# Kernel optimization log

Hardware: AMD Instinct MI355X
Metric: run time of the kernel (lower is better)

The kernel has to match this reference:

```python
import jax, jax.numpy as jnp
import numpy as np

B, S, H = 2, 2048, 1024
NH, HD = 16, 64  # num heads, head dim
EPS = 1e-12


def setup_inputs() -> dict:
    key = jax.random.key(0)
    ks = jax.random.split(key, 10)
    sc = 1.0 / np.sqrt(H)
    return {
        "hidden_states": jax.random.normal(ks[0], (B, S, H), jnp.float32),
        "Wq": jax.random.normal(ks[1], (H, H), jnp.float32) * sc,
        "bq": jnp.zeros((H,), jnp.float32),
        "Wk": jax.random.normal(ks[2], (H, H), jnp.float32) * sc,
        "bk": jnp.zeros((H,), jnp.float32),
        "Wv": jax.random.normal(ks[3], (H, H), jnp.float32) * sc,
        "bv": jnp.zeros((H,), jnp.float32),
        "Wo": jax.random.normal(ks[4], (H, H), jnp.float32) * sc,
        "bo": jnp.zeros((H,), jnp.float32),
        "ln_g": jnp.ones((H,), jnp.float32),
        "ln_b": jnp.zeros((H,), jnp.float32),
    }


def reference(hidden_states, Wq, bq, Wk, bk, Wv, bv, Wo, bo, ln_g, ln_b):
    x = hidden_states  # [B,S,H]
    def split_heads(t):
        return t.reshape(B, S, NH, HD).transpose(0, 2, 1, 3)  # [B,NH,S,HD]
    q = split_heads(x @ Wq.T + bq)
    k = split_heads(x @ Wk.T + bk)
    v = split_heads(x @ Wv.T + bv)
    scores = jnp.einsum("bhqd,bhkd->bhqk", q, k) / np.sqrt(HD)
    causal = jnp.tril(jnp.ones((S, S), bool))  # [S,S]
    scores = jnp.where(causal[None, None], scores, -jnp.inf)
    probs = jax.nn.softmax(scores, axis=-1)
    ctx = jnp.einsum("bhqk,bhkd->bhqd", probs, v)
    ctx = ctx.transpose(0, 2, 1, 3).reshape(B, S, H)
    attn_out = ctx @ Wo.T + bo
    y = attn_out + x
    mu = jnp.mean(y, axis=-1, keepdims=True)
    var = jnp.mean((y - mu) ** 2, axis=-1, keepdims=True)
    return (y - mu) / jnp.sqrt(var + EPS) * ln_g + ln_b
```

## Files before the change

kernel.cpp:

```cpp
#include <hip/hip_runtime.h>

#define B_  2
#define S_  2048
#define H_  1024
#define NH_ 16
#define HD_ 64
#define M_  (B_*S_)

typedef __attribute__((ext_vector_type(8))) __bf16 bf16x8;
typedef __attribute__((ext_vector_type(4))) float  f32x4;
typedef __attribute__((ext_vector_type(8))) unsigned short us8;
typedef __attribute__((ext_vector_type(4))) float  fl4;

__device__ __forceinline__ unsigned short f2bf(float f) {
    unsigned int u = __float_as_uint(f);
    u += 0x7fffu + ((u >> 16) & 1u);
    return (unsigned short)(u >> 16);
}

__global__ __launch_bounds__(256) void cast_kernel(
    const float* __restrict__ x,
    const float* __restrict__ wq, const float* __restrict__ wk,
    const float* __restrict__ wv, const float* __restrict__ wo,
    unsigned short* __restrict__ xb, unsigned short* __restrict__ wb) {
    size_t t  = (size_t)blockIdx.x * 256 + threadIdx.x;
    size_t e0 = t * 4;
    const size_t XN = (size_t)M_ * H_;
    const float* src;
    unsigned short* dst;
    if (e0 < XN) { src = x + e0; dst = xb + e0; }
    else {
        size_t j = e0 - XN;
        int w = (int)(j >> 20);
        size_t off = j & ((1u << 20) - 1);
        const float* wp = (w == 0) ? wq : (w == 1) ? wk : (w == 2) ? wv : wo;
        src = wp + off; dst = wb + j;
    }
    fl4 v = *(const fl4*)src;
    ushort4 o;
    o.x = f2bf(v.x); o.y = f2bf(v.y); o.z = f2bf(v.z); o.w = f2bf(v.w);
    *(ushort4*)dst = o;
}

__global__ __launch_bounds__(512) void gemm_qkv(
    const unsigned short* __restrict__ xb, const unsigned short* __restrict__ wb,
    const float* __restrict__ bq, const float* __restrict__ bk,
    const float* __restrict__ bv,
    unsigned short* __restrict__ qb, unsigned short* __restrict__ kbuf,
    unsigned short* __restrict__ vT) {
    __shared__ __align__(16) unsigned short As[128 * 72];
    __shared__ __align__(16) unsigned short Bs[128 * 72];
    const int z = blockIdx.z;
    const unsigned short* W = wb + ((size_t)z << 20);
    const int m0 = blockIdx.x * 128, n0 = blockIdx.y * 128;
    const int t = threadIdx.x, lane = t & 63, w = t >> 6;
    const int wm = w >> 2, wn = w & 3;
    const int quad = lane >> 4, l16 = lane & 15;
    const int sr = t >> 2, sc = (t & 3) * 16;
    const unsigned short* ga = xb + (size_t)(m0 + sr) * H_ + sc;
    const unsigned short* gb = W  + (size_t)(n0 + sr) * H_ + sc;

    us8 a0 = *(const us8*)(ga),     a1 = *(const us8*)(ga + 8);
    us8 b0 = *(const us8*)(gb),     b1 = *(const us8*)(gb + 8);

    f32x4 acc[4][2] = {};
    for (int k0 = 0; k0 < H_; k0 += 64) {
        if (k0) __syncthreads();
        *(us8*)&As[sr * 72 + sc]     = a0;  *(us8*)&As[sr * 72 + sc + 8] = a1;
        *(us8*)&Bs[sr * 72 + sc]     = b0;  *(us8*)&Bs[sr * 72 + sc + 8] = b1;
        __syncthreads();
        if (k0 + 64 < H_) {
            ga += 64; gb += 64;
            a0 = *(const us8*)(ga);  a1 = *(const us8*)(ga + 8);
            b0 = *(const us8*)(gb);  b1 = *(const us8*)(gb + 8);
        }
#pragma unroll
        for (int kk = 0; kk < 64; kk += 32) {
            bf16x8 af[4], bfr[2];
#pragma unroll
            for (int i = 0; i < 4; i++)
                af[i]  = *(const bf16x8*)&As[(wm * 64 + i * 16 + l16) * 72 + kk + quad * 8];
#pragma unroll
            for (int jn = 0; jn < 2; jn++)
                bfr[jn] = *(const bf16x8*)&Bs[(wn * 32 + jn * 16 + l16) * 72 + kk + quad * 8];
#pragma unroll
            for (int mi = 0; mi < 4; mi++)
#pragma unroll
                for (int ni = 0; ni < 2; ni++)
                    acc[mi][ni] = __builtin_amdgcn_mfma_f32_16x16x32_bf16(
                        af[mi], bfr[ni], acc[mi][ni], 0, 0, 0);
        }
    }
    const float* bias = (z == 0) ? bq : (z == 1) ? bk : bv;
    if (z == 2) {
#pragma unroll
        for (int mi = 0; mi < 4; mi++) {
#pragma unroll
            for (int ni = 0; ni < 2; ni++) {
                int col  = n0 + wn * 32 + ni * 16 + l16;
                float bval = bias[col];
                int row0 = m0 + wm * 64 + mi * 16 + quad * 4;
                int bb = row0 >> 11, s0 = row0 & 2047;
                ushort4 pk;
                pk.x = f2bf(acc[mi][ni][0] + bval);
                pk.y = f2bf(acc[mi][ni][1] + bval);
                pk.z = f2bf(acc[mi][ni][2] + bval);
                pk.w = f2bf(acc[mi][ni][3] + bval);
                *(ushort4*)&vT[((size_t)bb * NH_ * HD_ + col) * S_ + s0] = pk;
            }
        }
    } else {
        unsigned short* out = (z == 0) ? qb : kbuf;
        const float qs = (z == 0) ? 0.18033688f : 1.0f;
#pragma unroll
        for (int mi = 0; mi < 4; mi++) {
#pragma unroll
            for (int ni = 0; ni < 2; ni++) {
                int col = n0 + wn * 32 + ni * 16 + l16;
                float bval = bias[col];
#pragma unroll
                for (int r = 0; r < 4; r++) {
                    int row = m0 + wm * 64 + mi * 16 + quad * 4 + r;
                    out[(size_t)row * H_ + col] = f2bf((acc[mi][ni][r] + bval) * qs);
                }
            }
        }
    }
}

__global__ __launch_bounds__(512) void gemm_out(
    const unsigned short* __restrict__ ctxb, const unsigned short* __restrict__ wob,
    const float* __restrict__ bo, const float* __restrict__ x,
    float* __restrict__ y) {
    __shared__ __align__(16) unsigned short As[128 * 72];
    __shared__ __align__(16) unsigned short Bs[128 * 72];
    const int m0 = blockIdx.x * 128, n0 = blockIdx.y * 128;
    const int t = threadIdx.x, lane = t & 63, w = t >> 6;
    const int wm = w >> 2, wn = w & 3;
    const int quad = lane >> 4, l16 = lane & 15;
    const int sr = t >> 2, sc = (t & 3) * 16;
    const unsigned short* ga = ctxb + (size_t)(m0 + sr) * H_ + sc;
    const unsigned short* gb = wob  + (size_t)(n0 + sr) * H_ + sc;

    us8 a0 = *(const us8*)(ga),     a1 = *(const us8*)(ga + 8);
    us8 b0 = *(const us8*)(gb),     b1 = *(const us8*)(gb + 8);

    f32x4 acc[4][2] = {};
    for (int k0 = 0; k0 < H_; k0 += 64) {
        if (k0) __syncthreads();
        *(us8*)&As[sr * 72 + sc]     = a0;  *(us8*)&As[sr * 72 + sc + 8] = a1;
        *(us8*)&Bs[sr * 72 + sc]     = b0;  *(us8*)&Bs[sr * 72 + sc + 8] = b1;
        __syncthreads();
        if (k0 + 64 < H_) {
            ga += 64; gb += 64;
            a0 = *(const us8*)(ga);  a1 = *(const us8*)(ga + 8);
            b0 = *(const us8*)(gb);  b1 = *(const us8*)(gb + 8);
        }
#pragma unroll
        for (int kk = 0; kk < 64; kk += 32) {
            bf16x8 af[4], bfr[2];
#pragma unroll
            for (int i = 0; i < 4; i++)
                af[i]  = *(const bf16x8*)&As[(wm * 64 + i * 16 + l16) * 72 + kk + quad * 8];
#pragma unroll
            for (int jn = 0; jn < 2; jn++)
                bfr[jn] = *(const bf16x8*)&Bs[(wn * 32 + jn * 16 + l16) * 72 + kk + quad * 8];
#pragma unroll
            for (int mi = 0; mi < 4; mi++)
#pragma unroll
                for (int ni = 0; ni < 2; ni++)
                    acc[mi][ni] = __builtin_amdgcn_mfma_f32_16x16x32_bf16(
                        af[mi], bfr[ni], acc[mi][ni], 0, 0, 0);
        }
    }
#pragma unroll
    for (int mi = 0; mi < 4; mi++) {
#pragma unroll
        for (int ni = 0; ni < 2; ni++) {
            int col = n0 + wn * 32 + ni * 16 + l16;
            float bval = bo[col];
#pragma unroll
            for (int r = 0; r < 4; r++) {
                size_t idx = (size_t)(m0 + wm * 64 + mi * 16 + quad * 4 + r) * H_ + col;
                y[idx] = acc[mi][ni][r] + bval + x[idx];
            }
        }
    }
}

__global__ __launch_bounds__(512, 4) void attn_kernel(
    const unsigned short* __restrict__ qb, const unsigned short* __restrict__ kb,
    const unsigned short* __restrict__ vT, unsigned short* __restrict__ ctxb) {
    __shared__ __align__(16) unsigned short Ks[2][64 * 72];
    __shared__ __align__(16) unsigned short Vt[2][64 * 72];
    __shared__ __align__(16) unsigned short Ps[128 * 76];
    const int flat = blockIdx.x;
    const int xcd = flat & 7, slot = flat >> 3;
    const int bh  = xcd * 4 + (slot >> 4);
    const int p   = slot & 15;
    const int b = bh >> 4, h = bh & 15;
    const int t = threadIdx.x, lane = t & 63, wid = t >> 6;
    const int grp = wid >> 2, wid4 = wid & 3;
    const int quad = lane >> 4, l16 = lane & 15;
    const int sr8 = t >> 3, sc8 = (t & 7) * 8;
    const size_t headoff = (size_t)h * HD_;
    const unsigned short* vtb = vT + ((size_t)(b * NH_ + h) * HD_) * S_;

    const int qt = grp ? (31 - p) : p;
    const int q0 = qt * 64;
    const int nsteps = 32 - p;

    const size_t qr = (size_t)(b * S_ + q0 + wid4 * 16 + l16);
    bf16x8 qva = *(const bf16x8*)(qb + qr * H_ + headoff + quad * 8);
    bf16x8 qvb = *(const bf16x8*)(qb + qr * H_ + headoff + 32 + quad * 8);

    float m1 = -1e30f, l1 = 0.f;
    f32x4 o1[4] = {};

    const unsigned short* kptr = kb  + (size_t)(b * S_ + sr8) * H_ + headoff + sc8;
    const unsigned short* vptr = vtb + (size_t)sr8 * S_ + sc8;
    us8 nk = *(const us8*)kptr;
    us8 nv = *(const us8*)vptr;
    *(us8*)&Ks[0][sr8 * 72 + sc8] = nk;
    *(us8*)&Vt[0][sr8 * 72 + sc8] = nv;
    __syncthreads();

    for (int s = 0; s < nsteps; s++) {
        const int buf = s & 1;
        const bool pf = (s + 1 < nsteps);
        if (pf) {
            kptr += (size_t)64 * H_;
            vptr += 64;
            nk = *(const us8*)kptr;
            nv = *(const us8*)vptr;
        }
        if (s <= qt) {
            f32x4 sacc[4] = {};
#pragma unroll
            for (int kk = 0; kk < 64; kk += 32) {
                bf16x8 bqf = (kk == 0) ? qva : qvb;
#pragma unroll
                for (int nt = 0; nt < 4; nt++) {
                    bf16x8 ak = *(const bf16x8*)&Ks[buf][(nt * 16 + l16) * 72 + kk + quad * 8];
                    sacc[nt] = __builtin_amdgcn_mfma_f32_16x16x32_bf16(ak, bqf, sacc[nt], 0, 0, 0);
                }
            }
            if (s == qt) {
#pragma unroll
                for (int nt = 0; nt < 4; nt++) {
#pragma unroll
                    for (int r = 0; r < 4; r++) {
                        int key = nt * 16 + quad * 4 + r;
                        if (key > wid4 * 16 + l16) sacc[nt][r] = -1e30f;
                    }
                }
            }
            float mx = sacc[0][0];
#pragma unroll
            for (int nt = 0; nt < 4; nt++)
#pragma unroll
                for (int r = 0; r < 4; r++) mx = fmaxf(mx, sacc[nt][r]);
            mx = fmaxf(mx, __shfl_xor(mx, 16));
            mx = fmaxf(mx, __shfl_xor(mx, 32));
            float m_new = fmaxf(m1, mx);
            float alpha = __builtin_amdgcn_exp2f(m1 - m_new);
            float ss = 0.f;
#pragma unroll
            for (int nt = 0; nt < 4; nt++) {
                ushort4 pk;
                float p0 = __builtin_amdgcn_exp2f(sacc[nt][0] - m_new);
                float p1 = __builtin_amdgcn_exp2f(sacc[nt][1] - m_new);
                float p2 = __builtin_amdgcn_exp2f(sacc[nt][2] - m_new);
                float p3 = __builtin_amdgcn_exp2f(sacc[nt][3] - m_new);
                ss += (p0 + p1) + (p2 + p3);
                pk.x = (unsigned short)(__float_as_uint(p0) >> 16);
                pk.y = (unsigned short)(__float_as_uint(p1) >> 16);
                pk.z = (unsigned short)(__float_as_uint(p2) >> 16);
                pk.w = (unsigned short)(__float_as_uint(p3) >> 16);
                *(ushort4*)&Ps[(wid * 16 + l16) * 76 + nt * 16 + quad * 4] = pk;
            }
            ss += __shfl_xor(ss, 16);
            ss += __shfl_xor(ss, 32);
            l1 = l1 * alpha + ss;
            m1 = m_new;
#pragma unroll
            for (int dt = 0; dt < 4; dt++)
#pragma unroll
                for (int r = 0; r < 4; r++) o1[dt][r] *= alpha;
            __threadfence_block();
#pragma unroll
            for (int kk = 0; kk < 64; kk += 32) {
                bf16x8 pfr = *(const bf16x8*)&Ps[(wid * 16 + l16) * 76 + kk + quad * 8];
#pragma unroll
                for (int dt = 0; dt < 4; dt++) {
                    bf16x8 vf = *(const bf16x8*)&Vt[buf][(dt * 16 + l16) * 72 + kk + quad * 8];
                    o1[dt] = __builtin_amdgcn_mfma_f32_16x16x32_bf16(vf, pfr, o1[dt], 0, 0, 0);
                }
            }
        }
        if (pf) {
            *(us8*)&Ks[buf ^ 1][sr8 * 72 + sc8] = nk;
            *(us8*)&Vt[buf ^ 1][sr8 * 72 + sc8] = nv;
            __syncthreads();
        }
    }
    {
        const float inv = 1.0f / l1;
        size_t row = (size_t)(b * S_ + q0 + wid4 * 16 + l16);
#pragma unroll
        for (int dt = 0; dt < 4; dt++) {
            ushort4 pk;
            pk.x = f2bf(o1[dt][0] * inv);
            pk.y = f2bf(o1[dt][1] * inv);
            pk.z = f2bf(o1[dt][2] * inv);
            pk.w = f2bf(o1[dt][3] * inv);
            *(ushort4*)&ctxb[row * H_ + headoff + dt * 16 + quad * 4] = pk;
        }
    }
}

__global__ __launch_bounds__(256) void ln_kernel(
    const float* __restrict__ y, const float* __restrict__ g,
    const float* __restrict__ bta, float* __restrict__ out) {
    __shared__ float red[8];
    const int row = blockIdx.x, t = threadIdx.x;
    fl4 v = *(const fl4*)(y + (size_t)row * H_ + t * 4);
    float s  = v.x + v.y + v.z + v.w;
    float sq = v.x * v.x + v.y * v.y + v.z * v.z + v.w * v.w;
    for (int m = 1; m < 64; m <<= 1) { s += __shfl_xor(s, m); sq += __shfl_xor(sq, m); }
    const int wid = t >> 6, lane = t & 63;
    if (lane == 0) { red[wid * 2] = s; red[wid * 2 + 1] = sq; }
    __syncthreads();
    s  = red[0] + red[2] + red[4] + red[6];
    sq = red[1] + red[3] + red[5] + red[7];
    float mu   = s * (1.0f / H_);
    float var  = sq * (1.0f / H_) - mu * mu;
    float rstd = rsqrtf(fmaxf(var, 0.f) + 1e-12f);
    fl4 gg = *(const fl4*)(g + t * 4);
    fl4 bb = *(const fl4*)(bta + t * 4);
    fl4 o;
    o.x = (v.x - mu) * rstd * gg.x + bb.x;
    o.y = (v.y - mu) * rstd * gg.y + bb.y;
    o.z = (v.z - mu) * rstd * gg.z + bb.z;
    o.w = (v.w - mu) * rstd * gg.w + bb.w;
    *(fl4*)(out + (size_t)row * H_ + t * 4) = o;
}

extern "C" void kernel_launch(void* const* d_in, const int* in_sizes, int n_in,
                              void* d_out, int out_size, void* d_ws, size_t ws_size,
                              hipStream_t stream) {
    const float* x  = (const float*)d_in[0];
    const float* Wq = (const float*)d_in[1];
    const float* bq = (const float*)d_in[2];
    const float* Wk = (const float*)d_in[3];
    const float* bk = (const float*)d_in[4];
    const float* Wv = (const float*)d_in[5];
    const float* bv = (const float*)d_in[6];
    const float* Wo = (const float*)d_in[7];
    const float* bo = (const float*)d_in[8];
    const float* lg = (const float*)d_in[9];
    const float* lb = (const float*)d_in[10];
    float* out = (float*)d_out;

    const size_t MEG = 1024u * 1024u;
    unsigned short* ws16 = (unsigned short*)d_ws;
    unsigned short* xb   = ws16;
    unsigned short* wb   = ws16 + 4 * MEG;
    unsigned short* qb   = ws16 + 8 * MEG;
    unsigned short* kb   = ws16 + 12 * MEG;
    unsigned short* vT   = ws16 + 16 * MEG;
    unsigned short* ctxb = ws16 + 20 * MEG;
    float* y = (float*)(ws16 + 24 * MEG);

    cast_kernel<<<8192, 256, 0, stream>>>(x, Wq, Wk, Wv, Wo, xb, wb);
    gemm_qkv<<<dim3(32, 8, 3), 512, 0, stream>>>(xb, wb, bq, bk, bv, qb, kb, vT);
    attn_kernel<<<dim3(512), 512, 0, stream>>>(qb, kb, vT, ctxb);
    gemm_out<<<dim3(32, 8), 512, 0, stream>>>(ctxb, wb + 3 * MEG, bo, x, y);
    ln_kernel<<<4096, 256, 0, stream>>>(y, lg, lb, out);
}
```

Before: 198.4 us.

## Give each attention wave two 16-row query subtiles to reuse K/V fragments

The attention block shrinks from 8 waves to 4. Each wave now processes 32 query rows as two 16-row subtiles, so every K and V fragment read from LDS feeds two MFMAs instead of one. Each thread also loads twice as much K/V per tile step. The aim is to cut LDS read traffic and the number of waves per block in exchange for more registers per wave and fewer waves available to hide latency; launch bounds change from (512,4) to (256,2).

```diff
diff --git a/kernel.cpp b/kernel.cpp
--- a/kernel.cpp
+++ b/kernel.cpp
@@ -188,7 +188,7 @@
     }
 }
 
-__global__ __launch_bounds__(512, 4) void attn_kernel(
+__global__ __launch_bounds__(256, 2) void attn_kernel(
     const unsigned short* __restrict__ qb, const unsigned short* __restrict__ kb,
     const unsigned short* __restrict__ vT, unsigned short* __restrict__ ctxb) {
     __shared__ __align__(16) unsigned short Ks[2][64 * 72];
@@ -200,9 +200,9 @@
     const int p   = slot & 15;
     const int b = bh >> 4, h = bh & 15;
     const int t = threadIdx.x, lane = t & 63, wid = t >> 6;
-    const int grp = wid >> 2, wid4 = wid & 3;
+    const int grp = wid >> 1, whalf = wid & 1;
     const int quad = lane >> 4, l16 = lane & 15;
-    const int sr8 = t >> 3, sc8 = (t & 7) * 8;
+    const int sr = t >> 2, sc = (t & 3) * 16;
     const size_t headoff = (size_t)h * HD_;
     const unsigned short* vtb = vT + ((size_t)(b * NH_ + h) * HD_) * S_;
 
@@ -210,19 +210,23 @@
     const int q0 = qt * 64;
     const int nsteps = 32 - p;
 
-    const size_t qr = (size_t)(b * S_ + q0 + wid4 * 16 + l16);
-    bf16x8 qva = *(const bf16x8*)(qb + qr * H_ + headoff + quad * 8);
-    bf16x8 qvb = *(const bf16x8*)(qb + qr * H_ + headoff + 32 + quad * 8);
-
-    float m1 = -1e30f, l1 = 0.f;
-    f32x4 o1[4] = {};
-
-    const unsigned short* kptr = kb  + (size_t)(b * S_ + sr8) * H_ + headoff + sc8;
-    const unsigned short* vptr = vtb + (size_t)sr8 * S_ + sc8;
-    us8 nk = *(const us8*)kptr;
-    us8 nv = *(const us8*)vptr;
-    *(us8*)&Ks[0][sr8 * 72 + sc8] = nk;
-    *(us8*)&Vt[0][sr8 * 72 + sc8] = nv;
+    bf16x8 qv[2][2];
+#pragma unroll
+    for (int sub = 0; sub < 2; sub++) {
+        const size_t qr = (size_t)(b * S_ + q0 + whalf * 32 + sub * 16 + l16);
+        qv[sub][0] = *(const bf16x8*)(qb + qr * H_ + headoff + quad * 8);
+        qv[sub][1] = *(const bf16x8*)(qb + qr * H_ + headoff + 32 + quad * 8);
+    }
+
+    float mrun[2] = { -1e30f, -1e30f }, lrun[2] = { 0.f, 0.f };
+    f32x4 o[2][4] = {};
+
+    const unsigned short* kptr = kb  + (size_t)(b * S_ + sr) * H_ + headoff + sc;
+    const unsigned short* vptr = vtb + (size_t)sr * S_ + sc;
+    us8 nk0 = *(const us8*)kptr,       nk1 = *(const us8*)(kptr + 8);
+    us8 nv0 = *(const us8*)vptr,       nv1 = *(const us8*)(vptr + 8);
+    *(us8*)&Ks[0][sr * 72 + sc] = nk0;  *(us8*)&Ks[0][sr * 72 + sc + 8] = nk1;
+    *(us8*)&Vt[0][sr * 72 + sc] = nv0;  *(us8*)&Vt[0][sr * 72 + sc + 8] = nv1;
     __syncthreads();
 
     for (int s = 0; s < nsteps; s++) {
@@ -231,89 +235,97 @@
         if (pf) {
             kptr += (size_t)64 * H_;
             vptr += 64;
-            nk = *(const us8*)kptr;
-            nv = *(const us8*)vptr;
+            nk0 = *(const us8*)kptr;  nk1 = *(const us8*)(kptr + 8);
+            nv0 = *(const us8*)vptr;  nv1 = *(const us8*)(vptr + 8);
         }
         if (s <= qt) {
-            f32x4 sacc[4] = {};
+            f32x4 sacc[2][4] = {};
 #pragma unroll
             for (int kk = 0; kk < 64; kk += 32) {
-                bf16x8 bqf = (kk == 0) ? qva : qvb;
+                const int ki = kk >> 5;
 #pragma unroll
                 for (int nt = 0; nt < 4; nt++) {
                     bf16x8 ak = *(const bf16x8*)&Ks[buf][(nt * 16 + l16) * 72 + kk + quad * 8];
-                    sacc[nt] = __builtin_amdgcn_mfma_f32_16x16x32_bf16(ak, bqf, sacc[nt], 0, 0, 0);
-                }
-            }
-            if (s == qt) {
+                    sacc[0][nt] = __builtin_amdgcn_mfma_f32_16x16x32_bf16(ak, qv[0][ki], sacc[0][nt], 0, 0, 0);
+                    sacc[1][nt] = __builtin_amdgcn_mfma_f32_16x16x32_bf16(ak, qv[1][ki], sacc[1][nt], 0, 0, 0);
+                }
+            }
+#pragma unroll
+            for (int sub = 0; sub < 2; sub++) {
+                const int qrow = whalf * 32 + sub * 16 + l16;
+                if (s == qt) {
+#pragma unroll
+                    for (int nt = 0; nt < 4; nt++) {
+#pragma unroll
+                        for (int r = 0; r < 4; r++) {
+                            int key = nt * 16 + quad * 4 + r;
+                            if (key > qrow) sacc[sub][nt][r] = -1e30f;
+                        }
+                    }
+                }
+                float mx = sacc[sub][0][0];
+#pragma unroll
+                for (int nt = 0; nt < 4; nt++)
+#pragma unroll
+                    for (int r = 0; r < 4; r++) mx = fmaxf(mx, sacc[sub][nt][r]);
+                mx = fmaxf(mx, __shfl_xor(mx, 16));
+                mx = fmaxf(mx, __shfl_xor(mx, 32));
+                float m_new = fmaxf(mrun[sub], mx);
+                float alpha = __builtin_amdgcn_exp2f(mrun[sub] - m_new);
+                float ss = 0.f;
 #pragma unroll
                 for (int nt = 0; nt < 4; nt++) {
-#pragma unroll
-                    for (int r = 0; r < 4; r++) {
-                        int key = nt * 16 + quad * 4 + r;
-                        if (key > wid4 * 16 + l16) sacc[nt][r] = -1e30f;
-                    }
-                }
-            }
-            float mx = sacc[0][0];
-#pragma unroll
-            for (int nt = 0; nt < 4; nt++)
-#pragma unroll
-                for (int r = 0; r < 4; r++) mx = fmaxf(mx, sacc[nt][r]);
-            mx = fmaxf(mx, __shfl_xor(mx, 16));
-            mx = fmaxf(mx, __shfl_xor(mx, 32));
-            float m_new = fmaxf(m1, mx);
-            float alpha = __builtin_amdgcn_exp2f(m1 - m_new);
-            float ss = 0.f;
-#pragma unroll
-            for (int nt = 0; nt < 4; nt++) {
-                ushort4 pk;
-                float p0 = __builtin_amdgcn_exp2f(sacc[nt][0] - m_new);
-                float p1 = __builtin_amdgcn_exp2f(sacc[nt][1] - m_new);
-                float p2 = __builtin_amdgcn_exp2f(sacc[nt][2] - m_new);
-                float p3 = __builtin_amdgcn_exp2f(sacc[nt][3] - m_new);
-                ss += (p0 + p1) + (p2 + p3);
-                pk.x = (unsigned short)(__float_as_uint(p0) >> 16);
-                pk.y = (unsigned short)(__float_as_uint(p1) >> 16);
-                pk.z = (unsigned short)(__float_as_uint(p2) >> 16);
-                pk.w = (unsigned short)(__float_as_uint(p3) >> 16);
-                *(ushort4*)&Ps[(wid * 16 + l16) * 76 + nt * 16 + quad * 4] = pk;
-            }
-            ss += __shfl_xor(ss, 16);
-            ss += __shfl_xor(ss, 32);
-            l1 = l1 * alpha + ss;
-            m1 = m_new;
-#pragma unroll
-            for (int dt = 0; dt < 4; dt++)
-#pragma unroll
-                for (int r = 0; r < 4; r++) o1[dt][r] *= alpha;
+                    ushort4 pk;
+                    float p0 = __builtin_amdgcn_exp2f(sacc[sub][nt][0] - m_new);
+                    float p1 = __builtin_amdgcn_exp2f(sacc[sub][nt][1] - m_new);
+                    float p2 = __builtin_amdgcn_exp2f(sacc[sub][nt][2] - m_new);
+                    float p3 = __builtin_amdgcn_exp2f(sacc[sub][nt][3] - m_new);
+                    ss += (p0 + p1) + (p2 + p3);
+                    pk.x = (unsigned short)(__float_as_uint(p0) >> 16);
+                    pk.y = (unsigned short)(__float_as_uint(p1) >> 16);
+                    pk.z = (unsigned short)(__float_as_uint(p2) >> 16);
+                    pk.w = (unsigned short)(__float_as_uint(p3) >> 16);
+                    *(ushort4*)&Ps[(wid * 32 + sub * 16 + l16) * 76 + nt * 16 + quad * 4] = pk;
+                }
+                ss += __shfl_xor(ss, 16);
+                ss += __shfl_xor(ss, 32);
+                lrun[sub] = lrun[sub] * alpha + ss;
+                mrun[sub] = m_new;
+#pragma unroll
+                for (int dt = 0; dt < 4; dt++)
+#pragma unroll
+                    for (int r = 0; r < 4; r++) o[sub][dt][r] *= alpha;
+            }
             __threadfence_block();
 #pragma unroll
             for (int kk = 0; kk < 64; kk += 32) {
-                bf16x8 pfr = *(const bf16x8*)&Ps[(wid * 16 + l16) * 76 + kk + quad * 8];
+                bf16x8 pf0 = *(const bf16x8*)&Ps[(wid * 32 + l16) * 76 + kk + quad * 8];
+                bf16x8 pf1 = *(const bf16x8*)&Ps[(wid * 32 + 16 + l16) * 76 + kk + quad * 8];
 #pragma unroll
                 for (int dt = 0; dt < 4; dt++) {
                     bf16x8 vf = *(const bf16x8*)&Vt[buf][(dt * 16 + l16) * 72 + kk + quad * 8];
-                    o1[dt] = __builtin_amdgcn_mfma_f32_16x16x32_bf16(vf, pfr, o1[dt], 0, 0, 0);
+                    o[0][dt] = __builtin_amdgcn_mfma_f32_16x16x32_bf16(vf, pf0, o[0][dt], 0, 0, 0);
+                    o[1][dt] = __builtin_amdgcn_mfma_f32_16x16x32_bf16(vf, pf1, o[1][dt], 0, 0, 0);
                 }
             }
         }
         if (pf) {
-            *(us8*)&Ks[buf ^ 1][sr8 * 72 + sc8] = nk;
-            *(us8*)&Vt[buf ^ 1][sr8 * 72 + sc8] = nv;
+            *(us8*)&Ks[buf ^ 1][sr * 72 + sc] = nk0;  *(us8*)&Ks[buf ^ 1][sr * 72 + sc + 8] = nk1;
+            *(us8*)&Vt[buf ^ 1][sr * 72 + sc] = nv0;  *(us8*)&Vt[buf ^ 1][sr * 72 + sc + 8] = nv1;
             __syncthreads();
         }
     }
-    {
-        const float inv = 1.0f / l1;
-        size_t row = (size_t)(b * S_ + q0 + wid4 * 16 + l16);
+#pragma unroll
+    for (int sub = 0; sub < 2; sub++) {
+        const float inv = 1.0f / lrun[sub];
+        size_t row = (size_t)(b * S_ + q0 + whalf * 32 + sub * 16 + l16);
 #pragma unroll
         for (int dt = 0; dt < 4; dt++) {
             ushort4 pk;
-            pk.x = f2bf(o1[dt][0] * inv);
-            pk.y = f2bf(o1[dt][1] * inv);
-            pk.z = f2bf(o1[dt][2] * inv);
-            pk.w = f2bf(o1[dt][3] * inv);
+            pk.x = f2bf(o[sub][dt][0] * inv);
+            pk.y = f2bf(o[sub][dt][1] * inv);
+            pk.z = f2bf(o[sub][dt][2] * inv);
+            pk.w = f2bf(o[sub][dt][3] * inv);
             *(ushort4*)&ctxb[row * H_ + headoff + dt * 16 + quad * 4] = pk;
         }
     }
@@ -374,7 +386,7 @@
 
     cast_kernel<<<8192, 256, 0, stream>>>(x, Wq, Wk, Wv, Wo, xb, wb);
     gemm_qkv<<<dim3(32, 8, 3), 512, 0, stream>>>(xb, wb, bq, bk, bv, qb, kb, vT);
-    attn_kernel<<<dim3(512), 512, 0, stream>>>(qb, kb, vT, ctxb);
+    attn_kernel<<<dim3(512), 256, 0, stream>>>(qb, kb, vT, ctxb);
     gemm_out<<<dim3(32, 8), 512, 0, stream>>>(ctxb, wb + 3 * MEG, bo, x, y);
     ln_kernel<<<4096, 256, 0, stream>>>(y, lg, lb, out);
 }
```

Measured after the change: 210.7 us. 1.06x slower.
